# Optimization experiments

Measured on AMD Instinct MI355X. Metric: run time of the kernel, lower is better.

## Reference

```python
import jax, jax.numpy as jnp
import numpy as np

# Sparse MinkUNet-style backbone sizes
N0, N1, N2, N3 = 100000, 50000, 25000, 12500  # voxels per level (batch-concatenated)
K, KD = 27, 8        # 3x3x3 kernel offsets, stride-2 child offsets
B, S = 8, 1024       # batch, seed_num
C0, C1, C2, C3 = 32, 64, 128, 256
COUT = 512


def _w(k, shape, fan_in):
    return jax.random.normal(k, shape, dtype=jnp.float32) / np.sqrt(fan_in)


def setup_inputs() -> dict:
    key = jax.random.key(0)
    ks = jax.random.split(key, 32)
    inp = {}
    inp["feats"] = jax.random.normal(ks[0], (N0, 3), dtype=jnp.float32)
    # neighbor maps (kernel-offset gather indices, as built by a voxel hash map)
    inp["nbr0"] = jax.random.randint(ks[1], (N0, K), 0, N0, dtype=jnp.int32)
    inp["nbr1"] = jax.random.randint(ks[2], (N1, K), 0, N1, dtype=jnp.int32)
    inp["nbr2"] = jax.random.randint(ks[3], (N2, K), 0, N2, dtype=jnp.int32)
    inp["nbr3"] = jax.random.randint(ks[4], (N3, K), 0, N3, dtype=jnp.int32)
    # stride-2 downsample maps (coarse voxel -> fine children)
    inp["down1"] = jax.random.randint(ks[5], (N1, KD), 0, N0, dtype=jnp.int32)
    inp["down2"] = jax.random.randint(ks[6], (N2, KD), 0, N1, dtype=jnp.int32)
    inp["down3"] = jax.random.randint(ks[7], (N3, KD), 0, N2, dtype=jnp.int32)
    # nearest-parent upsample maps (fine voxel -> coarse parent)
    inp["up2"] = jax.random.randint(ks[8], (N2,), 0, N3, dtype=jnp.int32)
    inp["up1"] = jax.random.randint(ks[9], (N1,), 0, N2, dtype=jnp.int32)
    inp["up0"] = jax.random.randint(ks[10], (N0,), 0, N1, dtype=jnp.int32)
    # nearest-voxel devoxelize index for each FPS seed point
    inp["seed_idx"] = jax.random.randint(ks[11], (B, S), 0, N0, dtype=jnp.int32)
    # conv kernels [K, Cin, Cout] and 1x1 (linear) decoder weights
    inp["W_stem"] = _w(ks[12], (K, 3, C0), K * 3)
    inp["W_b0"] = _w(ks[13], (K, C0, C0), K * C0)
    inp["W_d1"] = _w(ks[14], (KD, C0, C1), KD * C0)
    inp["W_b1"] = _w(ks[15], (K, C1, C1), K * C1)
    inp["W_d2"] = _w(ks[16], (KD, C1, C2), KD * C1)
    inp["W_b2"] = _w(ks[17], (K, C2, C2), K * C2)
    inp["W_d3"] = _w(ks[18], (KD, C2, C3), KD * C2)
    inp["W_b3"] = _w(ks[19], (K, C3, C3), K * C3)
    inp["W_u2"] = _w(ks[20], (C3 + C2, 256), C3 + C2)
    inp["W_u1"] = _w(ks[21], (256 + C1, 128), 256 + C1)
    inp["W_u0"] = _w(ks[22], (128 + C0, 96), 128 + C0)
    inp["W_out"] = _w(ks[23], (96, COUT), 96)
    return inp


def sp_conv(f, nbr, W):
    # gather neighbor features then contract over (kernel offset, in-channel)
    g = f[nbr]                                # [N, K, Cin]
    return jnp.einsum('nkc,kco->no', g, W)    # [N, Cout]


def reference(feats, nbr0, nbr1, nbr2, nbr3, down1, down2, down3,
              up2, up1, up0, seed_idx,
              W_stem, W_b0, W_d1, W_b1, W_d2, W_b2, W_d3, W_b3,
              W_u2, W_u1, W_u0, W_out):
    relu = jax.nn.relu
    # encoder
    x0 = relu(sp_conv(feats, nbr0, W_stem))          # [N0, 32]
    x0 = x0 + relu(sp_conv(x0, nbr0, W_b0))
    x1 = relu(sp_conv(x0, down1, W_d1))              # [N1, 64]
    x1 = x1 + relu(sp_conv(x1, nbr1, W_b1))
    x2 = relu(sp_conv(x1, down2, W_d2))              # [N2, 128]
    x2 = x2 + relu(sp_conv(x2, nbr2, W_b2))
    x3 = relu(sp_conv(x2, down3, W_d3))              # [N3, 256]
    x3 = x3 + relu(sp_conv(x3, nbr3, W_b3))
    # decoder: nearest-parent upsample + skip concat + 1x1 conv
    u2 = relu(jnp.concatenate([x3[up2], x2], axis=-1) @ W_u2)   # [N2, 256]
    u1 = relu(jnp.concatenate([u2[up1], x1], axis=-1) @ W_u1)   # [N1, 128]
    u0 = relu(jnp.concatenate([u1[up0], x0], axis=-1) @ W_u0)   # [N0, 96]
    out_vox = u0 @ W_out                                        # [N0, 512]
    seed_feats = out_vox[seed_idx]                              # [B, S, 512]
    return jnp.transpose(seed_feats, (0, 2, 1))                 # [B, 512, S]
```

## Files before the change

### kernel.cpp

```cpp
#include <hip/hip_runtime.h>

typedef unsigned short u16;
typedef unsigned int u32;
typedef __bf16 bf16x8 __attribute__((ext_vector_type(8)));
typedef float f32x4 __attribute__((ext_vector_type(4)));

#define NV0 100000
#define NV1 50000
#define NV2 25000
#define NV3 12500

enum : long {
  OFF_WB0  = 0,
  OFF_WD1  = 27648,
  OFF_WB1  = 44032,
  OFF_WD2  = 154624,
  OFF_WB2  = 220160,
  OFF_WD3  = 662528,
  OFF_WB3  = 924672,
  OFF_WU2  = 2694144,
  OFF_WU1  = 2792448,
  OFF_WU0  = 2833408,
  OFF_WOUT = 2848768,
  OFF_TA   = 2897920,
  OFF_X0   = OFF_TA  + 3200000,
  OFF_X1   = OFF_X0  + 3200000,
  OFF_X2   = OFF_X1  + 3200000,
  OFF_X3   = OFF_X2  + 3200000,
  OFF_U2   = OFF_X3  + 3200000,
  OFF_U1   = OFF_U2  + 6400000,
  OFF_U0S  = OFF_U1  + 6400000,
  OFF_END  = OFF_U0S + 786432,
};

__device__ __forceinline__ float b2f(u16 u) {
  union { u32 i; float f; } x; x.i = ((u32)u) << 16; return x.f;
}
__device__ __forceinline__ u16 f2b(float f) {
  union { float f; u32 i; } x; x.f = f;
  u32 r = (x.i + 0x7FFFu + ((x.i >> 16) & 1u)) >> 16;
  return (u16)r;
}
__device__ __forceinline__ void gload16(const u16* g, const u16* l) {
  __builtin_amdgcn_global_load_lds(
      (const __attribute__((address_space(1))) void*)g,
      (__attribute__((address_space(3))) void*)(u16*)l, 16, 0, 0);
}
__device__ __forceinline__ void store_out(u16* p, float v)  { *p = f2b(v); }
__device__ __forceinline__ void store_out(float* p, float v) { *p = v; }
constexpr int ilog2c(int x) { return x <= 1 ? 0 : 1 + ilog2c(x / 2); }

struct PD { const float* src; u16* dst; int KK, CIN, COUT; };
struct PrepArgs { PD d[11]; };

__global__ __launch_bounds__(256) void prep_k(PrepArgs pa) {
  const PD d = pa.d[blockIdx.y];
  const int cc = d.CIN * d.COUT;
  const int total = d.KK * cc;
  for (int e = blockIdx.x * 256 + threadIdx.x; e < total; e += gridDim.x * 256) {
    int k = e / cc;
    int r = e - k * cc;
    int c = r / d.COUT;
    int o = r - c * d.COUT;
    d.dst[(k * d.COUT + o) * d.CIN + c] = f2b(d.src[e]);
  }
}

__global__ __launch_bounds__(256) void stem_k(const float* __restrict__ feats,
                                              const int* __restrict__ nbr0,
                                              const float* __restrict__ wstem,
                                              u16* __restrict__ out) {
  __shared__ float Wl[27 * 3 * 32];
  const int tid = threadIdx.x;
  for (int i = tid; i < 2592; i += 256) Wl[i] = wstem[i];
  __syncthreads();
  const int n = blockIdx.x * 8 + (tid >> 5);
  const int o = tid & 31;
  if (n >= NV0) return;
  float acc = 0.f;
  const int* nb = nbr0 + n * 27;
  #pragma unroll
  for (int k = 0; k < 27; k++) {
    const int iv = nb[k];
    const float* f = feats + iv * 3;
    acc = fmaf(f[0], Wl[(k * 3 + 0) * 32 + o], acc);
    acc = fmaf(f[1], Wl[(k * 3 + 1) * 32 + o], acc);
    acc = fmaf(f[2], Wl[(k * 3 + 2) * 32 + o], acc);
  }
  out[n * 32 + o] = f2b(fmaxf(acc, 0.f));
}

template <int BM, int BN, int WM, int WN, int COUTF, int KCT, int BK, int MODE,
          int CIN, int KK, int CA, bool RES, bool DORELU, typename OT>
__global__ __launch_bounds__(256, 4) void gemm_k(
    const u16* __restrict__ src0, const u16* __restrict__ src1,
    const int* __restrict__ idx0, const int* __restrict__ idx1,
    const u16* __restrict__ wt, const u16* __restrict__ base,
    OT* __restrict__ out, int N) {
  constexpr int NWM = BM / WM, NWN = BN / WN;
  static_assert(NWM * NWN == 4, "4 waves");
  constexpr int MI = WM / 16, NI = WN / 16;
  constexpr int CB = KCT - CA;
  constexpr int SLOTS = BK / 8;
  constexpr int SM = SLOTS - 1;
  constexpr int LSL = ilog2c(SLOTS);
  constexpr int RPC = 64 / SLOTS;
  constexpr int LRPC = ilog2c(RPC);
  constexpr int ACH = (BM * BK) / 512;
  constexpr int BCH = (BN * BK) / 512;
  constexpr int NIT = KCT / BK;
  constexpr int LOGC = ilog2c(CIN);
  constexpr int NIDX = (MODE == 0) ? BM * KK : (MODE == 1 ? BM : (MODE == 2 ? 2 * BM : 1));
  static_assert(KCT % BK == 0, "K mult of BK");
  static_assert(MODE != 1 || (CA % BK == 0), "concat boundary aligned");

  __shared__ u16 As[2][BM * BK];
  __shared__ u16 Bs[2][BN * BK];
  __shared__ int Is[NIDX];
  const int tid = threadIdx.x;
  const int w = tid >> 6, lane = tid & 63;
  const int quad = lane >> 4, l16 = lane & 15;
  const int wm = w % NWM, wn = w / NWM;
  const int row0 = blockIdx.x * BM;
  const int col0 = blockIdx.y * BN;
  const int Nm1 = N - 1;
  const int srow = lane >> LSL;
  const int g    = (lane & SM) ^ (srow & SM);
  const int cl   = g * 8;

  if constexpr (MODE == 0) {
    for (int e = tid; e < BM * KK; e += 256) {
      const int r = e / KK, k = e - r * KK;
      int n = row0 + r; n = (n > Nm1) ? Nm1 : n;
      Is[e] = idx0[(long)n * KK + k];
    }
  } else if constexpr (MODE == 1) {
    for (int e = tid; e < BM; e += 256) {
      int n = row0 + e; n = (n > Nm1) ? Nm1 : n;
      Is[e] = idx0[n];
    }
  } else if constexpr (MODE == 2) {
    for (int e = tid; e < BM; e += 256) {
      int n = row0 + e; n = (n > Nm1) ? Nm1 : n;
      const int s = idx0[n];
      Is[e] = idx1[s];
      Is[BM + e] = s;
    }
  }
  if constexpr (MODE != 3) __syncthreads();

  f32x4 acc[MI][NI];
  #pragma unroll
  for (int i = 0; i < MI; i++)
    #pragma unroll
    for (int j = 0; j < NI; j++) acc[i][j] = {0.f, 0.f, 0.f, 0.f};

  auto stage = [&](int buf, int kc0) {
    for (int c = w; c < ACH + BCH; c += 4) {
      const int cab = kc0 + cl;
      if (c < ACH) {
        const int r = (c << LRPC) + srow;
        const u16* gp;
        if constexpr (MODE == 0) {
          const int k = cab >> LOGC;
          gp = src0 + (long)Is[r * KK + k] * CIN + (cab & (CIN - 1));
        } else if constexpr (MODE == 1) {
          if (kc0 < CA) gp = src0 + (long)Is[r] * CA + cab;
          else {
            int n = row0 + r; n = (n > Nm1) ? Nm1 : n;
            gp = src1 + (long)n * CB + (cab - CA);
          }
        } else if constexpr (MODE == 2) {
          if (kc0 < CA) gp = src0 + (long)Is[r] * CA + cab;
          else          gp = src1 + (long)Is[BM + r] * CB + (cab - CA);
        } else {
          int n = row0 + r; n = (n > Nm1) ? Nm1 : n;
          gp = src0 + (long)n * KCT + cab;
        }
        gload16(gp, &As[buf][c * 512]);
      } else {
        const int cb = c - ACH;
        const int o = col0 + (cb << LRPC) + srow;
        const u16* gp;
        if constexpr (MODE == 0) {
          const int k = cab >> LOGC;
          gp = wt + ((long)(k * COUTF + o)) * CIN + (cab & (CIN - 1));
        } else {
          gp = wt + (long)o * KCT + cab;
        }
        gload16(gp, &Bs[buf][cb * 512]);
      }
    }
  };

  stage(0, 0);
  #pragma unroll 1
  for (int it = 0; it < NIT; it++) {
    __syncthreads();
    if (it + 1 < NIT) stage((it + 1) & 1, (it + 1) * BK);
    const int buf = it & 1;
    #pragma unroll
    for (int kk = 0; kk < BK / 32; kk++) {
      bf16x8 af[MI], bfr[NI];
      #pragma unroll
      for (int i = 0; i < MI; i++) {
        const int row = wm * WM + i * 16 + l16;
        const int slot = row * SLOTS + (((kk << 2) + quad) ^ (row & SM));
        af[i] = *(const bf16x8*)&As[buf][slot * 8];
      }
      #pragma unroll
      for (int j = 0; j < NI; j++) {
        const int row = wn * WN + j * 16 + l16;
        const int slot = row * SLOTS + (((kk << 2) + quad) ^ (row & SM));
        bfr[j] = *(const bf16x8*)&Bs[buf][slot * 8];
      }
      #pragma unroll
      for (int i = 0; i < MI; i++)
        #pragma unroll
        for (int j = 0; j < NI; j++)
          acc[i][j] = __builtin_amdgcn_mfma_f32_16x16x32_bf16(af[i], bfr[j], acc[i][j], 0, 0, 0);
    }
  }

  #pragma unroll
  for (int i = 0; i < MI; i++) {
    #pragma unroll
    for (int j = 0; j < NI; j++) {
      const int col = col0 + wn * WN + j * 16 + l16;
      #pragma unroll
      for (int r = 0; r < 4; r++) {
        const int n = row0 + wm * WM + i * 16 + quad * 4 + r;
        if (n < N) {
          float v = acc[i][j][r];
          if constexpr (RES)         v = b2f(base[(long)n * COUTF + col]) + fmaxf(v, 0.f);
          else if constexpr (DORELU) v = fmaxf(v, 0.f);
          store_out(&out[(long)n * COUTF + col], v);
        }
      }
    }
  }
}

__global__ __launch_bounds__(256) void tout_k(const float* __restrict__ tmp,
                                              float* __restrict__ outp) {
  __shared__ float tl[64][65];
  const int tid = threadIdx.x;
  const int r0 = blockIdx.x * 64, o0 = blockIdx.y * 64;
  {
    const int rl = tid >> 2, oc = (tid & 3) * 16;
    const float* src = &tmp[(r0 + rl) * 512 + o0 + oc];
    #pragma unroll
    for (int j = 0; j < 16; j++) tl[rl][oc + j] = src[j];
  }
  __syncthreads();
  {
    const int ol = tid >> 2, sc = (tid & 3) * 16;
    const int b = r0 >> 10, s0 = r0 & 1023;
    float* dst = &outp[((long)b * 512 + (o0 + ol)) * 1024 + s0 + sc];
    #pragma unroll
    for (int j = 0; j < 16; j++) dst[j] = tl[sc + j][ol];
  }
}

extern "C" void kernel_launch(void* const* d_in, const int* in_sizes, int n_in,
                              void* d_out, int out_size, void* d_ws, size_t ws_size,
                              hipStream_t stream) {
  const float* feats = (const float*)d_in[0];
  const int* nbr0  = (const int*)d_in[1];
  const int* nbr1  = (const int*)d_in[2];
  const int* nbr2  = (const int*)d_in[3];
  const int* nbr3  = (const int*)d_in[4];
  const int* down1 = (const int*)d_in[5];
  const int* down2 = (const int*)d_in[6];
  const int* down3 = (const int*)d_in[7];
  const int* up2   = (const int*)d_in[8];
  const int* up1   = (const int*)d_in[9];
  const int* up0   = (const int*)d_in[10];
  const int* seed  = (const int*)d_in[11];
  u16* ws = (u16*)d_ws;

  PrepArgs pa;
  pa.d[0]  = {(const float*)d_in[13], ws + OFF_WB0,  27, 32, 32};
  pa.d[1]  = {(const float*)d_in[14], ws + OFF_WD1,  8,  32, 64};
  pa.d[2]  = {(const float*)d_in[15], ws + OFF_WB1,  27, 64, 64};
  pa.d[3]  = {(const float*)d_in[16], ws + OFF_WD2,  8,  64, 128};
  pa.d[4]  = {(const float*)d_in[17], ws + OFF_WB2,  27, 128, 128};
  pa.d[5]  = {(const float*)d_in[18], ws + OFF_WD3,  8,  128, 256};
  pa.d[6]  = {(const float*)d_in[19], ws + OFF_WB3,  27, 256, 256};
  pa.d[7]  = {(const float*)d_in[20], ws + OFF_WU2,  1,  384, 256};
  pa.d[8]  = {(const float*)d_in[21], ws + OFF_WU1,  1,  320, 128};
  pa.d[9]  = {(const float*)d_in[22], ws + OFF_WU0,  1,  160, 96};
  pa.d[10] = {(const float*)d_in[23], ws + OFF_WOUT, 1,  96,  512};
  prep_k<<<dim3(128, 11), 256, 0, stream>>>(pa);

  u16* ta  = ws + OFF_TA;
  u16* x0  = ws + OFF_X0;
  u16* x1  = ws + OFF_X1;
  u16* x2  = ws + OFF_X2;
  u16* x3  = ws + OFF_X3;
  u16* u2b = ws + OFF_U2;
  u16* u1b = ws + OFF_U1;
  u16* u0s = ws + OFF_U0S;
  float* tmp = (float*)(ws + OFF_TA);

  stem_k<<<12500, 256, 0, stream>>>(feats, nbr0, (const float*)d_in[12], ta);

  gemm_k<128, 32, 32, 32, 32, 864, 32, 0, 32, 27, 0, true, true, u16>
      <<<dim3(782, 1), 256, 0, stream>>>(ta, nullptr, nbr0, nullptr, ws + OFF_WB0, ta, x0, NV0);
  gemm_k<64, 64, 32, 32, 64, 256, 64, 0, 32, 8, 0, false, true, u16>
      <<<dim3(782, 1), 256, 0, stream>>>(x0, nullptr, down1, nullptr, ws + OFF_WD1, nullptr, ta, NV1);
  gemm_k<64, 64, 32, 32, 64, 1728, 64, 0, 64, 27, 0, true, true, u16>
      <<<dim3(782, 1), 256, 0, stream>>>(ta, nullptr, nbr1, nullptr, ws + OFF_WB1, ta, x1, NV1);
  gemm_k<64, 64, 32, 32, 128, 512, 64, 0, 64, 8, 0, false, true, u16>
      <<<dim3(391, 2), 256, 0, stream>>>(x1, nullptr, down2, nullptr, ws + OFF_WD2, nullptr, ta, NV2);
  gemm_k<64, 64, 32, 32, 128, 3456, 64, 0, 128, 27, 0, true, true, u16>
      <<<dim3(391, 2), 256, 0, stream>>>(ta, nullptr, nbr2, nullptr, ws + OFF_WB2, ta, x2, NV2);
  gemm_k<64, 64, 32, 32, 256, 1024, 64, 0, 128, 8, 0, false, true, u16>
      <<<dim3(196, 4), 256, 0, stream>>>(x2, nullptr, down3, nullptr, ws + OFF_WD3, nullptr, ta, NV3);
  gemm_k<64, 64, 32, 32, 256, 6912, 64, 0, 256, 27, 0, true, true, u16>
      <<<dim3(196, 4), 256, 0, stream>>>(ta, nullptr, nbr3, nullptr, ws + OFF_WB3, ta, x3, NV3);
  gemm_k<64, 64, 32, 32, 256, 384, 64, 1, 32, 1, 256, false, true, u16>
      <<<dim3(391, 4), 256, 0, stream>>>(x3, x2, up2, nullptr, ws + OFF_WU2, nullptr, u2b, NV2);
  gemm_k<64, 64, 32, 32, 128, 320, 64, 1, 32, 1, 256, false, true, u16>
      <<<dim3(782, 2), 256, 0, stream>>>(u2b, x1, up1, nullptr, ws + OFF_WU1, nullptr, u1b, NV1);
  gemm_k<64, 96, 32, 48, 96, 160, 32, 2, 32, 1, 128, false, true, u16>
      <<<dim3(128, 1), 256, 0, stream>>>(u1b, x0, seed, up0, ws + OFF_WU0, nullptr, u0s, 8192);
  gemm_k<64, 64, 32, 32, 512, 96, 32, 3, 32, 1, 0, false, false, float>
      <<<dim3(128, 8), 256, 0, stream>>>(u0s, nullptr, nullptr, nullptr, ws + OFF_WOUT, nullptr, tmp, 8192);
  tout_k<<<dim3(128, 8), 256, 0, stream>>>(tmp, (float*)d_out);
}
```

Before: 533.3 us.

## Split-K the level-2/3 sparse convs and precompute gather offsets in staging

Splits the reduction of the two deepest 27-offset sparse convolutions across two blocks via blockIdx.z. Each half writes fp32 partials, and a new fix kernel sums them and applies relu plus the residual. The aim is more blocks in flight on those small-N layers, at the cost of extra fp32 partial traffic and one more launch per layer. It also precomputes per-thread gather offsets and pre-scales the shared-memory indices by channel count, which cuts the integer address arithmetic in the staging loop.

```diff
diff --git a/kernel.cpp b/kernel.cpp
--- a/kernel.cpp
+++ b/kernel.cpp
@@ -4,6 +4,7 @@
 typedef unsigned int u32;
 typedef __bf16 bf16x8 __attribute__((ext_vector_type(8)));
 typedef float f32x4 __attribute__((ext_vector_type(4)));
+typedef u16 u16x4 __attribute__((ext_vector_type(4)));
 
 #define NV0 100000
 #define NV1 50000
@@ -91,7 +92,7 @@
 }
 
 template <int BM, int BN, int WM, int WN, int COUTF, int KCT, int BK, int MODE,
-          int CIN, int KK, int CA, bool RES, bool DORELU, typename OT>
+          int CIN, int KK, int CA, int KSPL, bool RES, bool DORELU, typename OT>
 __global__ __launch_bounds__(256, 4) void gemm_k(
     const u16* __restrict__ src0, const u16* __restrict__ src1,
     const int* __restrict__ idx0, const int* __restrict__ idx1,
@@ -108,11 +109,15 @@
   constexpr int LRPC = ilog2c(RPC);
   constexpr int ACH = (BM * BK) / 512;
   constexpr int BCH = (BN * BK) / 512;
-  constexpr int NIT = KCT / BK;
+  constexpr int NIT = KCT / BK / KSPL;
   constexpr int LOGC = ilog2c(CIN);
-  constexpr int NIDX = (MODE == 0) ? BM * KK : (MODE == 1 ? BM : (MODE == 2 ? 2 * BM : 1));
-  static_assert(KCT % BK == 0, "K mult of BK");
-  static_assert(MODE != 1 || (CA % BK == 0), "concat boundary aligned");
+  constexpr int ATRIPS = ACH / 4;
+  constexpr int CTRIPS = (ACH + BCH + 3) / 4;
+  constexpr int NIDX = (MODE == 0) ? BM * KK : (MODE == 3 ? 1 : 2 * BM);
+  static_assert(ACH % 4 == 0, "A chunks divisible by wave count");
+  static_assert(KCT % (BK * KSPL) == 0, "K mult of BK*KSPL");
+  static_assert((MODE != 1 && MODE != 2) || (CA % BK == 0), "concat boundary aligned");
+  static_assert(KSPL == 1 || MODE == 0, "split only for sparse conv");
 
   __shared__ u16 As[2][BM * BK];
   __shared__ u16 Bs[2][BN * BK];
@@ -132,23 +137,48 @@
     for (int e = tid; e < BM * KK; e += 256) {
       const int r = e / KK, k = e - r * KK;
       int n = row0 + r; n = (n > Nm1) ? Nm1 : n;
-      Is[e] = idx0[(long)n * KK + k];
+      Is[e] = idx0[(long)n * KK + k] * CIN;
     }
   } else if constexpr (MODE == 1) {
     for (int e = tid; e < BM; e += 256) {
       int n = row0 + e; n = (n > Nm1) ? Nm1 : n;
-      Is[e] = idx0[n];
+      Is[e] = idx0[n] * CA;
+      Is[BM + e] = n * CB;
     }
   } else if constexpr (MODE == 2) {
     for (int e = tid; e < BM; e += 256) {
       int n = row0 + e; n = (n > Nm1) ? Nm1 : n;
       const int s = idx0[n];
-      Is[e] = idx1[s];
-      Is[BM + e] = s;
+      Is[e] = idx1[s] * CA;
+      Is[BM + e] = s * CB;
     }
   }
   if constexpr (MODE != 3) __syncthreads();
 
+  int pre[CTRIPS];
+  #pragma unroll
+  for (int t = 0; t < CTRIPS; t++) {
+    const int c = w + 4 * t;
+    if (t < ATRIPS) {
+      const int r = (c << LRPC) + srow;
+      if constexpr (MODE == 0) {
+        pre[t] = (r * KK + (cl >> LOGC)) * 4;
+      } else if constexpr (MODE == 3) {
+        int n = row0 + r; n = (n > Nm1) ? Nm1 : n;
+        pre[t] = n * KCT + cl;
+      } else {
+        pre[t] = r * 4;
+      }
+    } else if (c < ACH + BCH) {
+      const int o = col0 + ((c - ACH) << LRPC) + srow;
+      if constexpr (MODE == 0)
+        pre[t] = (cl >> LOGC) * (COUTF * CIN) + o * CIN + (cl & (CIN - 1));
+      else
+        pre[t] = o * KCT + cl;
+    }
+  }
+  const int claneA = (MODE == 0) ? (cl & (CIN - 1)) : cl;
+
   f32x4 acc[MI][NI];
   #pragma unroll
   for (int i = 0; i < MI; i++)
@@ -156,48 +186,40 @@
     for (int j = 0; j < NI; j++) acc[i][j] = {0.f, 0.f, 0.f, 0.f};
 
   auto stage = [&](int buf, int kc0) {
-    for (int c = w; c < ACH + BCH; c += 4) {
-      const int cab = kc0 + cl;
-      if (c < ACH) {
-        const int r = (c << LRPC) + srow;
-        const u16* gp;
-        if constexpr (MODE == 0) {
-          const int k = cab >> LOGC;
-          gp = src0 + (long)Is[r * KK + k] * CIN + (cab & (CIN - 1));
-        } else if constexpr (MODE == 1) {
-          if (kc0 < CA) gp = src0 + (long)Is[r] * CA + cab;
-          else {
-            int n = row0 + r; n = (n > Nm1) ? Nm1 : n;
-            gp = src1 + (long)n * CB + (cab - CA);
-          }
-        } else if constexpr (MODE == 2) {
-          if (kc0 < CA) gp = src0 + (long)Is[r] * CA + cab;
-          else          gp = src1 + (long)Is[BM + r] * CB + (cab - CA);
-        } else {
-          int n = row0 + r; n = (n > Nm1) ? Nm1 : n;
-          gp = src0 + (long)n * KCT + cab;
-        }
-        gload16(gp, &As[buf][c * 512]);
+    int kadd = 0, cadd = 0, kcc = 0;
+    const u16* sA = src0;
+    if constexpr (MODE == 0) {
+      kadd = (kc0 >> LOGC) * 4;
+      cadd = kc0 & (CIN - 1);
+      kcc  = (kc0 >> LOGC) * (COUTF * CIN) + cadd;
+    } else if constexpr (MODE == 1 || MODE == 2) {
+      if (kc0 >= CA) { kadd = BM * 4; cadd = kc0 - CA; sA = src1; }
+      else           { cadd = kc0; }
+    }
+    #pragma unroll
+    for (int t = 0; t < CTRIPS; t++) {
+      const int c = w + 4 * t;
+      if constexpr (CTRIPS * 4 > ACH + BCH) { if (c >= ACH + BCH) continue; }
+      if (t < ATRIPS) {
+        int off;
+        if constexpr (MODE == 3) off = pre[t] + kc0;
+        else off = *(const int*)((const char*)Is + (pre[t] + kadd)) + cadd + claneA;
+        gload16(sA + off, &As[buf][c * 512]);
       } else {
-        const int cb = c - ACH;
-        const int o = col0 + (cb << LRPC) + srow;
-        const u16* gp;
-        if constexpr (MODE == 0) {
-          const int k = cab >> LOGC;
-          gp = wt + ((long)(k * COUTF + o)) * CIN + (cab & (CIN - 1));
-        } else {
-          gp = wt + (long)o * KCT + cab;
-        }
-        gload16(gp, &Bs[buf][cb * 512]);
+        int off;
+        if constexpr (MODE == 0) off = pre[t] + kcc;
+        else                     off = pre[t] + kc0;
+        gload16(wt + off, &Bs[buf][(c - ACH) * 512]);
       }
     }
   };
 
-  stage(0, 0);
+  const int kb = (KSPL > 1) ? (int)blockIdx.z * (KCT / KSPL) : 0;
+  stage(0, kb);
   #pragma unroll 1
   for (int it = 0; it < NIT; it++) {
     __syncthreads();
-    if (it + 1 < NIT) stage((it + 1) & 1, (it + 1) * BK);
+    if (it + 1 < NIT) stage((it + 1) & 1, kb + (it + 1) * BK);
     const int buf = it & 1;
     #pragma unroll
     for (int kk = 0; kk < BK / 32; kk++) {
@@ -222,6 +244,8 @@
     }
   }
 
+  OT* op = out;
+  if constexpr (KSPL > 1) op += (long)blockIdx.z * ((long)N * COUTF);
   #pragma unroll
   for (int i = 0; i < MI; i++) {
     #pragma unroll
@@ -234,11 +258,25 @@
           float v = acc[i][j][r];
           if constexpr (RES)         v = b2f(base[(long)n * COUTF + col]) + fmaxf(v, 0.f);
           else if constexpr (DORELU) v = fmaxf(v, 0.f);
-          store_out(&out[(long)n * COUTF + col], v);
+          store_out(&op[(long)n * COUTF + col], v);
         }
       }
     }
   }
+}
+
+__global__ __launch_bounds__(256) void fix_k(const float* __restrict__ p0,
+                                             const float* __restrict__ p1,
+                                             const u16* __restrict__ base,
+                                             u16* __restrict__ out) {
+  const long i = ((long)blockIdx.x * 256 + threadIdx.x) * 4;
+  const f32x4 a = *(const f32x4*)(p0 + i);
+  const f32x4 b = *(const f32x4*)(p1 + i);
+  const u16x4 bs = *(const u16x4*)(base + i);
+  u16x4 r;
+  #pragma unroll
+  for (int j = 0; j < 4; j++) r[j] = f2b(b2f(bs[j]) + fmaxf(a[j] + b[j], 0.f));
+  *(u16x4*)(out + i) = r;
 }
 
 __global__ __launch_bounds__(256) void tout_k(const float* __restrict__ tmp,
@@ -301,31 +339,34 @@
   u16* u2b = ws + OFF_U2;
   u16* u1b = ws + OFF_U1;
   u16* u0s = ws + OFF_U0S;
-  float* tmp = (float*)(ws + OFF_TA);
+  float* tmp  = (float*)(ws + OFF_TA);
+  float* part = (float*)(ws + OFF_U2);
 
   stem_k<<<12500, 256, 0, stream>>>(feats, nbr0, (const float*)d_in[12], ta);
 
-  gemm_k<128, 32, 32, 32, 32, 864, 32, 0, 32, 27, 0, true, true, u16>
+  gemm_k<128, 32, 32, 32, 32, 864, 32, 0, 32, 27, 0, 1, true, true, u16>
       <<<dim3(782, 1), 256, 0, stream>>>(ta, nullptr, nbr0, nullptr, ws + OFF_WB0, ta, x0, NV0);
-  gemm_k<64, 64, 32, 32, 64, 256, 64, 0, 32, 8, 0, false, true, u16>
+  gemm_k<64, 64, 32, 32, 64, 256, 64, 0, 32, 8, 0, 1, false, true, u16>
       <<<dim3(782, 1), 256, 0, stream>>>(x0, nullptr, down1, nullptr, ws + OFF_WD1, nullptr, ta, NV1);
-  gemm_k<64, 64, 32, 32, 64, 1728, 64, 0, 64, 27, 0, true, true, u16>
+  gemm_k<64, 64, 32, 32, 64, 1728, 64, 0, 64, 27, 0, 1, true, true, u16>
       <<<dim3(782, 1), 256, 0, stream>>>(ta, nullptr, nbr1, nullptr, ws + OFF_WB1, ta, x1, NV1);
-  gemm_k<64, 64, 32, 32, 128, 512, 64, 0, 64, 8, 0, false, true, u16>
+  gemm_k<64, 64, 32, 32, 128, 512, 64, 0, 64, 8, 0, 1, false, true, u16>
       <<<dim3(391, 2), 256, 0, stream>>>(x1, nullptr, down2, nullptr, ws + OFF_WD2, nullptr, ta, NV2);
-  gemm_k<64, 64, 32, 32, 128, 3456, 64, 0, 128, 27, 0, true, true, u16>
-      <<<dim3(391, 2), 256, 0, stream>>>(ta, nullptr, nbr2, nullptr, ws + OFF_WB2, ta, x2, NV2);
-  gemm_k<64, 64, 32, 32, 256, 1024, 64, 0, 128, 8, 0, false, true, u16>
+  gemm_k<64, 64, 32, 32, 128, 3456, 64, 0, 128, 27, 0, 2, false, false, float>
+      <<<dim3(391, 2, 2), 256, 0, stream>>>(ta, nullptr, nbr2, nullptr, ws + OFF_WB2, nullptr, part, NV2);
+  fix_k<<<dim3(3125), 256, 0, stream>>>(part, part + 3200000, ta, x2);
+  gemm_k<64, 64, 32, 32, 256, 1024, 64, 0, 128, 8, 0, 1, false, true, u16>
       <<<dim3(196, 4), 256, 0, stream>>>(x2, nullptr, down3, nullptr, ws + OFF_WD3, nullptr, ta, NV3);
-  gemm_k<64, 64, 32, 32, 256, 6912, 64, 0, 256, 27, 0, true, true, u16>
-      <<<dim3(196, 4), 256, 0, stream>>>(ta, nullptr, nbr3, nullptr, ws + OFF_WB3, ta, x3, NV3);
-  gemm_k<64, 64, 32, 32, 256, 384, 64, 1, 32, 1, 256, false, true, u16>
+  gemm_k<64, 64, 32, 32, 256, 6912, 64, 0, 256, 27, 0, 2, false, false, float>
+      <<<dim3(196, 4, 2), 256, 0, stream>>>(ta, nullptr, nbr3, nullptr, ws + OFF_WB3, nullptr, part, NV3);
+  fix_k<<<dim3(3125), 256, 0, stream>>>(part, part + 3200000, ta, x3);
+  gemm_k<64, 64, 32, 32, 256, 384, 64, 1, 32, 1, 256, 1, false, true, u16>
       <<<dim3(391, 4), 256, 0, stream>>>(x3, x2, up2, nullptr, ws + OFF_WU2, nullptr, u2b, NV2);
-  gemm_k<64, 64, 32, 32, 128, 320, 64, 1, 32, 1, 256, false, true, u16>
+  gemm_k<64, 64, 32, 32, 128, 320, 64, 1, 32, 1, 256, 1, false, true, u16>
       <<<dim3(782, 2), 256, 0, stream>>>(u2b, x1, up1, nullptr, ws + OFF_WU1, nullptr, u1b, NV1);
-  gemm_k<64, 96, 32, 48, 96, 160, 32, 2, 32, 1, 128, false, true, u16>
+  gemm_k<64, 96, 32, 48, 96, 160, 32, 2, 32, 1, 128, 1, false, true, u16>
       <<<dim3(128, 1), 256, 0, stream>>>(u1b, x0, seed, up0, ws + OFF_WU0, nullptr, u0s, 8192);
-  gemm_k<64, 64, 32, 32, 512, 96, 32, 3, 32, 1, 0, false, false, float>
+  gemm_k<64, 64, 32, 32, 512, 96, 32, 3, 32, 1, 0, 1, false, false, float>
       <<<dim3(128, 8), 256, 0, stream>>>(u0s, nullptr, nullptr, nullptr, ws + OFF_WOUT, nullptr, tmp, 8192);
   tout_k<<<dim3(128, 8), 256, 0, stream>>>(tmp, (float*)d_out);
 }
```

New measurement: 495.6 us. 1.08x faster.
